# Kernel optimization log

Hardware: AMD Instinct MI355X
Metric: run time of the kernel (lower is better)

## Reference

```python
import jax, jax.numpy as jnp
import numpy as np

B, T, C, H = 2, 2048, 1024, 16
D = C // H  # head dim = 64


def setup_inputs() -> dict:
    key = jax.random.key(0)
    ks = jax.random.split(key, 9)
    x = jax.random.normal(ks[0], (B, T, C), dtype=jnp.float32)
    # causal mask: True above the diagonal => positions to mask out
    mask = jnp.triu(jnp.ones((T, T), dtype=bool), k=1)[None, None]  # [1,1,T,T]
    s = 0.02
    Wq = jax.random.normal(ks[1], (C, C), dtype=jnp.float32) * s
    Wk = jax.random.normal(ks[2], (C, C), dtype=jnp.float32) * s
    Wv = jax.random.normal(ks[3], (C, C), dtype=jnp.float32) * s
    Wo = jax.random.normal(ks[4], (C, C), dtype=jnp.float32) * s
    bq = jax.random.normal(ks[5], (C,), dtype=jnp.float32) * s
    bk = jax.random.normal(ks[6], (C,), dtype=jnp.float32) * s
    bv = jax.random.normal(ks[7], (C,), dtype=jnp.float32) * s
    bo = jax.random.normal(ks[8], (C,), dtype=jnp.float32) * s
    return {"x": x, "mask": mask, "Wq": Wq, "bq": bq, "Wk": Wk, "bk": bk,
            "Wv": Wv, "bv": bv, "Wo": Wo, "bo": bo}


def reference(x, mask, Wq, bq, Wk, bk, Wv, bv, Wo, bo):
    b, t, c = x.shape
    # QKV projections, split heads -> [B,H,T,D]
    q = (x @ Wq + bq).reshape(b, t, H, D).transpose(0, 2, 1, 3)
    k = (x @ Wk + bk).reshape(b, t, H, D).transpose(0, 2, 1, 3)
    v = (x @ Wv + bv).reshape(b, t, H, D).transpose(0, 2, 1, 3)
    # scaled dot-product scores [B,H,T,T]
    att = jnp.einsum('bhtd,bhsd->bhts', q, k) * (1.0 / jnp.sqrt(jnp.float32(D)))
    att = jnp.where(mask, jnp.float32(-jnp.inf), att)
    att = jax.nn.softmax(att, axis=-1)  # dropout p=0.0 -> identity
    y = jnp.einsum('bhts,bhsd->bhtd', att, v)  # [B,H,T,D]
    y = y.transpose(0, 2, 1, 3).reshape(b, t, c)
    return y @ Wo + bo
```

## Files before the change

kernel.cpp:

```cpp
#include <hip/hip_runtime.h>
#include <hip/hip_bf16.h>

#define BB 2
#define TT 2048
#define CC 1024
#define HH 16
#define DD 64
#define MM (BB*TT)

typedef float f32x4 __attribute__((ext_vector_type(4)));
typedef __bf16 bf16x8 __attribute__((ext_vector_type(8)));
typedef unsigned int u32x4 __attribute__((ext_vector_type(4)));
typedef unsigned int u32x2 __attribute__((ext_vector_type(2)));

__device__ __forceinline__ unsigned short f2bf(float f) {
    unsigned int u = __float_as_uint(f);
    u += 0x7fff + ((u >> 16) & 1);
    return (unsigned short)(u >> 16);
}
__device__ __forceinline__ unsigned int pk2(float a, float b) {
    return (unsigned int)f2bf(a) | ((unsigned int)f2bf(b) << 16);
}

__global__ __launch_bounds__(256) void cvt_f32_bf16(
    const float* __restrict__ in, unsigned short* __restrict__ out)
{
    const size_t i = (size_t)blockIdx.x * 256 + threadIdx.x;
    const float4* in4 = (const float4*)in;
    float4 a = in4[2 * i], b = in4[2 * i + 1];
    u32x4 o;
    o[0] = pk2(a.x, a.y); o[1] = pk2(a.z, a.w);
    o[2] = pk2(b.x, b.y); o[3] = pk2(b.z, b.w);
    *(u32x4*)(out + 8 * i) = o;
}

__global__ __launch_bounds__(256) void wtrans_kernel(
    const float* __restrict__ W0, const float* __restrict__ W1,
    const float* __restrict__ W2, const float* __restrict__ W3,
    unsigned short* __restrict__ wt)
{
    const int tid = threadIdx.x;
    const int n0 = blockIdx.x * 64;
    const int k0 = blockIdx.y * 64;
    const int which = blockIdx.z;
    const float* W = (which == 0) ? W0 : (which == 1) ? W1 : (which == 2) ? W2 : W3;

    __shared__ float t_lds[64][68];

    #pragma unroll
    for (int p = 0; p < 4; ++p) {
        int idx = tid + p * 256;
        int r   = idx >> 4;
        int c4  = (idx & 15) * 4;
        *(float4*)&t_lds[r][c4] = *(const float4*)(W + (size_t)(k0 + r) * CC + n0 + c4);
    }
    __syncthreads();

    const int nl = tid >> 2;
    const int ks = (tid & 3) * 16;
    unsigned int w[8];
    #pragma unroll
    for (int j = 0; j < 8; ++j)
        w[j] = pk2(t_lds[ks + 2 * j][nl], t_lds[ks + 2 * j + 1][nl]);
    unsigned short* dst = wt + (size_t)which * CC * CC + (size_t)(n0 + nl) * CC + k0 + ks;
    u32x4 o0; o0[0] = w[0]; o0[1] = w[1]; o0[2] = w[2]; o0[3] = w[3];
    u32x4 o1; o1[0] = w[4]; o1[1] = w[5]; o1[2] = w[6]; o1[3] = w[7];
    *(u32x4*)dst = o0;
    *(u32x4*)(dst + 8) = o1;
}

__global__ __launch_bounds__(256) void gemm_qkv_mfma(
    const unsigned short* __restrict__ xbf, const unsigned short* __restrict__ wt,
    const float* __restrict__ bq, const float* __restrict__ bk, const float* __restrict__ bv,
    unsigned short* __restrict__ qbf, unsigned short* __restrict__ kbf,
    unsigned short* __restrict__ vtbf)
{
    const int tid = threadIdx.x;
    const int m0 = blockIdx.y * 128;
    const int nc0 = blockIdx.x * 128;
    const int which = nc0 >> 10;
    const int cb = nc0 & 1023;
    const unsigned short* Bt = wt + (size_t)which * CC * CC;
    const float* bias = (which == 0) ? bq : (which == 1) ? bk : bv;

    __shared__ unsigned short lds_a[128][40];
    __shared__ unsigned short lds_b[128][40];

    const int lane = tid & 63;
    const int wv = tid >> 6;
    const int wm = (wv & 1) * 64;
    const int wn = (wv >> 1) * 64;
    const int fr = lane & 15;
    const int ks = lane >> 4;

    f32x4 acc[4][4];
    #pragma unroll
    for (int i = 0; i < 4; ++i)
        #pragma unroll
        for (int j = 0; j < 4; ++j) { acc[i][j][0]=0.f; acc[i][j][1]=0.f; acc[i][j][2]=0.f; acc[i][j][3]=0.f; }

    for (int k0 = 0; k0 < CC; k0 += 32) {
        __syncthreads();
        #pragma unroll
        for (int p = 0; p < 2; ++p) {
            int c = tid + p * 256;
            int row = c >> 2, slot = c & 3;
            *(u32x4*)&lds_a[row][slot * 8] =
                *(const u32x4*)(xbf + (size_t)(m0 + row) * CC + k0 + slot * 8);
            *(u32x4*)&lds_b[row][slot * 8] =
                *(const u32x4*)(Bt + (size_t)(cb + row) * CC + k0 + slot * 8);
        }
        __syncthreads();

        bf16x8 af[4], bfv[4];
        #pragma unroll
        for (int i = 0; i < 4; ++i) {
            af[i]  = __builtin_bit_cast(bf16x8, *(const u32x4*)&lds_a[wm + i * 16 + fr][ks * 8]);
            bfv[i] = __builtin_bit_cast(bf16x8, *(const u32x4*)&lds_b[wn + i * 16 + fr][ks * 8]);
        }
        #pragma unroll
        for (int mi = 0; mi < 4; ++mi)
            #pragma unroll
            for (int ni = 0; ni < 4; ++ni)
                acc[mi][ni] = __builtin_amdgcn_mfma_f32_16x16x32_bf16(af[mi], bfv[ni], acc[mi][ni], 0, 0, 0);
    }

    #pragma unroll
    for (int ni = 0; ni < 4; ++ni) {
        const int c = cb + wn + ni * 16 + fr;
        const float bv2 = bias[c];
        const int h = c >> 6, d = c & 63;
        #pragma unroll
        for (int mi = 0; mi < 4; ++mi) {
            const int mb = m0 + wm + mi * 16 + ks * 4;
            const int b = mb >> 11, t = mb & 2047;
            if (which == 2) {
                u32x2 pkd;
                pkd[0] = pk2(acc[mi][ni][0] + bv2, acc[mi][ni][1] + bv2);
                pkd[1] = pk2(acc[mi][ni][2] + bv2, acc[mi][ni][3] + bv2);
                *(u32x2*)(vtbf + (((size_t)(b * HH + h) * DD + d) * TT) + t) = pkd;
            } else {
                unsigned short* dst = (which == 0) ? qbf : kbf;
                const float scl = (which == 0) ? 0.125f : 1.0f;
                #pragma unroll
                for (int j = 0; j < 4; ++j)
                    dst[(((size_t)(b * HH + h) * TT + (t + j)) * DD) + d] =
                        f2bf((acc[mi][ni][j] + bv2) * scl);
            }
        }
    }
}

__global__ __launch_bounds__(256) void attn_mfma(
    const unsigned short* __restrict__ qbf, const unsigned short* __restrict__ kbf,
    const unsigned short* __restrict__ vtbf, unsigned short* __restrict__ ybf)
{
    const int tid  = threadIdx.x;
    const int w    = tid >> 6;
    const int lane = tid & 63;
    const int g    = lane >> 4;
    const int i    = lane & 15;
    const int qi   = 31 - (int)blockIdx.x;
    const int h    = blockIdx.y;
    const int b    = blockIdx.z;
    const int q0   = qi * 64;
    const size_t hq = (size_t)(b * HH + h) * TT * DD;
    const size_t hv = (size_t)(b * HH + h) * DD * TT;

    __shared__ __align__(16) unsigned short k_lds[64][72];
    __shared__ __align__(16) unsigned short vt_lds[64][72];
    __shared__ __align__(16) unsigned short p_lds[64][72];

    bf16x8 qf[2];
    {
        const unsigned short* qrow = qbf + hq + (size_t)(q0 + 16 * w + i) * DD + g * 8;
        qf[0] = __builtin_bit_cast(bf16x8, *(const u32x4*)qrow);
        qf[1] = __builtin_bit_cast(bf16x8, *(const u32x4*)(qrow + 32));
    }

    f32x4 o_acc[4];
    f32x4 m_i, l_i;
    #pragma unroll
    for (int ni = 0; ni < 4; ++ni) { o_acc[ni][0]=0.f; o_acc[ni][1]=0.f; o_acc[ni][2]=0.f; o_acc[ni][3]=0.f; }
    #pragma unroll
    for (int e = 0; e < 4; ++e) { m_i[e] = -1e30f; l_i[e] = 0.f; }

    for (int kk = 0; kk <= qi; ++kk) {
        const int s0 = kk * 64;
        __syncthreads();
        #pragma unroll
        for (int p = 0; p < 2; ++p) {
            int c = tid + p * 256;
            int row = c >> 3, slot = c & 7;
            *(u32x4*)&k_lds[row][slot * 8] =
                *(const u32x4*)(kbf + hq + (size_t)(s0 + row) * DD + slot * 8);
            *(u32x4*)&vt_lds[row][slot * 8] =
                *(const u32x4*)(vtbf + hv + (size_t)row * TT + s0 + slot * 8);
        }
        __syncthreads();

        f32x4 s_acc[4];
        #pragma unroll
        for (int ni = 0; ni < 4; ++ni) { s_acc[ni][0]=0.f; s_acc[ni][1]=0.f; s_acc[ni][2]=0.f; s_acc[ni][3]=0.f; }
        #pragma unroll
        for (int ks = 0; ks < 2; ++ks)
            #pragma unroll
            for (int ni = 0; ni < 4; ++ni) {
                bf16x8 kb = __builtin_bit_cast(bf16x8,
                    *(const u32x4*)&k_lds[ni * 16 + i][ks * 32 + g * 8]);
                s_acc[ni] = __builtin_amdgcn_mfma_f32_16x16x32_bf16(qf[ks], kb, s_acc[ni], 0, 0, 0);
            }

        if (kk == qi) {
            #pragma unroll
            for (int ni = 0; ni < 4; ++ni)
                #pragma unroll
                for (int reg = 0; reg < 4; ++reg)
                    if (ni * 16 + i > 16 * w + 4 * g + reg) s_acc[ni][reg] = -1e30f;
        }

        f32x4 rmax = s_acc[0];
        #pragma unroll
        for (int ni = 1; ni < 4; ++ni)
            #pragma unroll
            for (int e = 0; e < 4; ++e) rmax[e] = fmaxf(rmax[e], s_acc[ni][e]);
        #pragma unroll
        for (int msk = 1; msk < 16; msk <<= 1)
            #pragma unroll
            for (int e = 0; e < 4; ++e) rmax[e] = fmaxf(rmax[e], __shfl_xor(rmax[e], msk));

        f32x4 m_new, alpha;
        #pragma unroll
        for (int e = 0; e < 4; ++e) {
            m_new[e] = fmaxf(m_i[e], rmax[e]);
            alpha[e] = __expf(m_i[e] - m_new[e]);
        }
        f32x4 rsum;
        #pragma unroll
        for (int e = 0; e < 4; ++e) rsum[e] = 0.f;
        #pragma unroll
        for (int ni = 0; ni < 4; ++ni)
            #pragma unroll
            for (int e = 0; e < 4; ++e) {
                float pv = __expf(s_acc[ni][e] - m_new[e]);
                s_acc[ni][e] = pv;
                rsum[e] += pv;
            }
        #pragma unroll
        for (int msk = 1; msk < 16; msk <<= 1)
            #pragma unroll
            for (int e = 0; e < 4; ++e) rsum[e] += __shfl_xor(rsum[e], msk);
        #pragma unroll
        for (int e = 0; e < 4; ++e) {
            l_i[e] = l_i[e] * alpha[e] + rsum[e];
            m_i[e] = m_new[e];
        }
        #pragma unroll
        for (int ni = 0; ni < 4; ++ni)
            #pragma unroll
            for (int e = 0; e < 4; ++e) o_acc[ni][e] *= alpha[e];

        #pragma unroll
        for (int ni = 0; ni < 4; ++ni)
            #pragma unroll
            for (int reg = 0; reg < 4; ++reg)
                p_lds[16 * w + 4 * g + reg][ni * 16 + i] = f2bf(s_acc[ni][reg]);

        #pragma unroll
        for (int ks = 0; ks < 2; ++ks) {
            bf16x8 pa = __builtin_bit_cast(bf16x8,
                *(const u32x4*)&p_lds[16 * w + i][ks * 32 + g * 8]);
            #pragma unroll
            for (int ni = 0; ni < 4; ++ni) {
                bf16x8 vb = __builtin_bit_cast(bf16x8,
                    *(const u32x4*)&vt_lds[ni * 16 + i][ks * 32 + g * 8]);
                o_acc[ni] = __builtin_amdgcn_mfma_f32_16x16x32_bf16(pa, vb, o_acc[ni], 0, 0, 0);
            }
        }
    }

    f32x4 inv;
    #pragma unroll
    for (int e = 0; e < 4; ++e) inv[e] = 1.0f / l_i[e];
    #pragma unroll
    for (int ni = 0; ni < 4; ++ni)
        #pragma unroll
        for (int reg = 0; reg < 4; ++reg)
            ybf[((size_t)b * TT + (q0 + 16 * w + 4 * g + reg)) * CC + h * DD + ni * 16 + i] =
                f2bf(o_acc[ni][reg] * inv[reg]);
}

__global__ __launch_bounds__(256) void gemm_out_mfma(
    const unsigned short* __restrict__ ybf, const unsigned short* __restrict__ wt_o,
    const float* __restrict__ bo, float* __restrict__ out)
{
    const int tid = threadIdx.x;
    const int m0 = blockIdx.y * 128;
    const int n0 = blockIdx.x * 128;

    __shared__ unsigned short lds_a[128][40];
    __shared__ unsigned short lds_b[128][40];

    const int lane = tid & 63;
    const int wv = tid >> 6;
    const int wm = (wv & 1) * 64;
    const int wn = (wv >> 1) * 64;
    const int fr = lane & 15;
    const int ks = lane >> 4;

    f32x4 acc[4][4];
    #pragma unroll
    for (int i = 0; i < 4; ++i)
        #pragma unroll
        for (int j = 0; j < 4; ++j) { acc[i][j][0]=0.f; acc[i][j][1]=0.f; acc[i][j][2]=0.f; acc[i][j][3]=0.f; }

    for (int k0 = 0; k0 < CC; k0 += 32) {
        __syncthreads();
        #pragma unroll
        for (int p = 0; p < 2; ++p) {
            int c = tid + p * 256;
            int row = c >> 2, slot = c & 3;
            *(u32x4*)&lds_a[row][slot * 8] =
                *(const u32x4*)(ybf + (size_t)(m0 + row) * CC + k0 + slot * 8);
            *(u32x4*)&lds_b[row][slot * 8] =
                *(const u32x4*)(wt_o + (size_t)(n0 + row) * CC + k0 + slot * 8);
        }
        __syncthreads();

        bf16x8 af[4], bfv[4];
        #pragma unroll
        for (int i = 0; i < 4; ++i) {
            af[i]  = __builtin_bit_cast(bf16x8, *(const u32x4*)&lds_a[wm + i * 16 + fr][ks * 8]);
            bfv[i] = __builtin_bit_cast(bf16x8, *(const u32x4*)&lds_b[wn + i * 16 + fr][ks * 8]);
        }
        #pragma unroll
        for (int mi = 0; mi < 4; ++mi)
            #pragma unroll
            for (int ni = 0; ni < 4; ++ni)
                acc[mi][ni] = __builtin_amdgcn_mfma_f32_16x16x32_bf16(af[mi], bfv[ni], acc[mi][ni], 0, 0, 0);
    }

    #pragma unroll
    for (int ni = 0; ni < 4; ++ni) {
        const int n = n0 + wn + ni * 16 + fr;
        const float bv2 = bo[n];
        #pragma unroll
        for (int mi = 0; mi < 4; ++mi) {
            #pragma unroll
            for (int j = 0; j < 4; ++j) {
                const int m = m0 + wm + mi * 16 + ks * 4 + j;
                out[(size_t)m * CC + n] = acc[mi][ni][j] + bv2;
            }
        }
    }
}

extern "C" void kernel_launch(void* const* d_in, const int* in_sizes, int n_in,
                              void* d_out, int out_size, void* d_ws, size_t ws_size,
                              hipStream_t stream) {
    const float* x  = (const float*)d_in[0];
    const float* Wq = (const float*)d_in[2];
    const float* bq = (const float*)d_in[3];
    const float* Wk = (const float*)d_in[4];
    const float* bk = (const float*)d_in[5];
    const float* Wv = (const float*)d_in[6];
    const float* bv = (const float*)d_in[7];
    const float* Wo = (const float*)d_in[8];
    const float* bo = (const float*)d_in[9];
    float* out = (float*)d_out;

    const size_t NE = (size_t)MM * CC;
    unsigned short* xbf  = (unsigned short*)d_ws;
    unsigned short* ybf  = xbf + NE;
    unsigned short* wt   = ybf + NE;
    unsigned short* qbf  = wt + (size_t)4 * CC * CC;
    unsigned short* kbf  = qbf + NE;
    unsigned short* vtbf = kbf + NE;

    cvt_f32_bf16<<<2048, 256, 0, stream>>>(x, xbf);
    wtrans_kernel<<<dim3(16, 16, 4), 256, 0, stream>>>(Wq, Wk, Wv, Wo, wt);
    gemm_qkv_mfma<<<dim3(24, 32), 256, 0, stream>>>(
        xbf, wt, bq, bk, bv, qbf, kbf, vtbf);
    attn_mfma<<<dim3(TT / 64, HH, BB), 256, 0, stream>>>(qbf, kbf, vtbf, ybf);
    gemm_out_mfma<<<dim3(8, 32), 256, 0, stream>>>(
        ybf, wt + (size_t)3 * CC * CC, bo, out);
}
```

Baseline: 296.0 us.

## Use direct global-to-LDS loads in GEMMs and 128-row attention tiles with prefetch

Both GEMMs now fill LDS with global_load_lds instead of loading through registers, and drop the padding so each 16-byte row segment is contiguous. This can add LDS bank conflicts on the fragment reads. The attention kernel now runs 512 threads over 128 query rows, so each K/V tile loaded into LDS serves twice as many queries. It also prefetches the next K/V tile into registers while computing the current one, and lets the first four waves skip the final diagonal tile. The larger block and LDS footprint may lower occupancy and leave waves idle on that last tile.

Result: faster. 273.5 us (-7.6%).

```diff
diff --git a/kernel.cpp b/kernel.cpp
--- a/kernel.cpp
+++ b/kernel.cpp
@@ -20,6 +20,13 @@
 }
 __device__ __forceinline__ unsigned int pk2(float a, float b) {
     return (unsigned int)f2bf(a) | ((unsigned int)f2bf(b) << 16);
+}
+
+__device__ __forceinline__ void gload_lds16(const void* g, void* l) {
+    __builtin_amdgcn_global_load_lds(
+        (const __attribute__((address_space(1))) unsigned int*)(unsigned long long)g,
+        (__attribute__((address_space(3))) unsigned int*)(unsigned int)(unsigned long long)l,
+        16, 0, 0);
 }
 
 __global__ __launch_bounds__(256) void cvt_f32_bf16(
@@ -83,8 +90,8 @@
     const unsigned short* Bt = wt + (size_t)which * CC * CC;
     const float* bias = (which == 0) ? bq : (which == 1) ? bk : bv;
 
-    __shared__ unsigned short lds_a[128][40];
-    __shared__ unsigned short lds_b[128][40];
+    __shared__ __align__(16) unsigned short lds_a[128][32];
+    __shared__ __align__(16) unsigned short lds_b[128][32];
 
     const int lane = tid & 63;
     const int wv = tid >> 6;
@@ -93,6 +100,9 @@
     const int fr = lane & 15;
     const int ks = lane >> 4;
 
+    const int lrow = lane >> 2;
+    const int lcol = (lane & 3) * 8;
+
     f32x4 acc[4][4];
     #pragma unroll
     for (int i = 0; i < 4; ++i)
@@ -102,13 +112,10 @@
     for (int k0 = 0; k0 < CC; k0 += 32) {
         __syncthreads();
         #pragma unroll
-        for (int p = 0; p < 2; ++p) {
-            int c = tid + p * 256;
-            int row = c >> 2, slot = c & 3;
-            *(u32x4*)&lds_a[row][slot * 8] =
-                *(const u32x4*)(xbf + (size_t)(m0 + row) * CC + k0 + slot * 8);
-            *(u32x4*)&lds_b[row][slot * 8] =
-                *(const u32x4*)(Bt + (size_t)(cb + row) * CC + k0 + slot * 8);
+        for (int c = 0; c < 2; ++c) {
+            const int r0 = (wv * 2 + c) * 16;
+            gload_lds16(xbf + (size_t)(m0 + r0 + lrow) * CC + k0 + lcol, &lds_a[r0][0]);
+            gload_lds16(Bt  + (size_t)(cb + r0 + lrow) * CC + k0 + lcol, &lds_b[r0][0]);
         }
         __syncthreads();
 
@@ -151,7 +158,7 @@
     }
 }
 
-__global__ __launch_bounds__(256) void attn_mfma(
+__global__ __launch_bounds__(512) void attn_mfma(
     const unsigned short* __restrict__ qbf, const unsigned short* __restrict__ kbf,
     const unsigned short* __restrict__ vtbf, unsigned short* __restrict__ ybf)
 {
@@ -160,16 +167,16 @@
     const int lane = tid & 63;
     const int g    = lane >> 4;
     const int i    = lane & 15;
-    const int qi   = 31 - (int)blockIdx.x;
+    const int qi   = 15 - (int)blockIdx.x;
     const int h    = blockIdx.y;
     const int b    = blockIdx.z;
-    const int q0   = qi * 64;
+    const int q0   = qi * 128;
     const size_t hq = (size_t)(b * HH + h) * TT * DD;
     const size_t hv = (size_t)(b * HH + h) * DD * TT;
 
     __shared__ __align__(16) unsigned short k_lds[64][72];
     __shared__ __align__(16) unsigned short vt_lds[64][72];
-    __shared__ __align__(16) unsigned short p_lds[64][72];
+    __shared__ __align__(16) unsigned short p_lds[128][72];
 
     bf16x8 qf[2];
     {
@@ -185,38 +192,48 @@
     #pragma unroll
     for (int e = 0; e < 4; ++e) { m_i[e] = -1e30f; l_i[e] = 0.f; }
 
-    for (int kk = 0; kk <= qi; ++kk) {
+    const int srow  = tid >> 3;
+    const int sslot = (tid & 7) * 8;
+
+    const int nt = 2 * qi + 2;
+    u32x4 kreg = *(const u32x4*)(kbf + hq + (size_t)srow * DD + sslot);
+    u32x4 vreg = *(const u32x4*)(vtbf + hv + (size_t)srow * TT + sslot);
+
+    for (int kk = 0; kk < nt; ++kk) {
+        __syncthreads();
+        *(u32x4*)&k_lds[srow][sslot]  = kreg;
+        *(u32x4*)&vt_lds[srow][sslot] = vreg;
+        __syncthreads();
+        if (kk + 1 < nt) {
+            const int s1 = (kk + 1) * 64;
+            kreg = *(const u32x4*)(kbf + hq + (size_t)(s1 + srow) * DD + sslot);
+            vreg = *(const u32x4*)(vtbf + hv + (size_t)srow * TT + s1 + sslot);
+        }
+
+        if (kk == nt - 1 && w < 4) continue;
+
         const int s0 = kk * 64;
-        __syncthreads();
-        #pragma unroll
-        for (int p = 0; p < 2; ++p) {
-            int c = tid + p * 256;
-            int row = c >> 3, slot = c & 7;
-            *(u32x4*)&k_lds[row][slot * 8] =
-                *(const u32x4*)(kbf + hq + (size_t)(s0 + row) * DD + slot * 8);
-            *(u32x4*)&vt_lds[row][slot * 8] =
-                *(const u32x4*)(vtbf + hv + (size_t)row * TT + s0 + slot * 8);
-        }
-        __syncthreads();
-
         f32x4 s_acc[4];
         #pragma unroll
         for (int ni = 0; ni < 4; ++ni) { s_acc[ni][0]=0.f; s_acc[ni][1]=0.f; s_acc[ni][2]=0.f; s_acc[ni][3]=0.f; }
         #pragma unroll
-        for (int ks = 0; ks < 2; ++ks)
+        for (int lks = 0; lks < 2; ++lks)
             #pragma unroll
             for (int ni = 0; ni < 4; ++ni) {
                 bf16x8 kb = __builtin_bit_cast(bf16x8,
-                    *(const u32x4*)&k_lds[ni * 16 + i][ks * 32 + g * 8]);
-                s_acc[ni] = __builtin_amdgcn_mfma_f32_16x16x32_bf16(qf[ks], kb, s_acc[ni], 0, 0, 0);
-            }
-
-        if (kk == qi) {
-            #pragma unroll
-            for (int ni = 0; ni < 4; ++ni)
+                    *(const u32x4*)&k_lds[ni * 16 + i][lks * 32 + g * 8]);
+                s_acc[ni] = __builtin_amdgcn_mfma_f32_16x16x32_bf16(qf[lks], kb, s_acc[ni], 0, 0, 0);
+            }
+
+        if (kk >= 2 * qi) {
+            const int r_glob = q0 + 16 * w + 4 * g;
+            #pragma unroll
+            for (int ni = 0; ni < 4; ++ni) {
+                const int s_glob = s0 + ni * 16 + i;
                 #pragma unroll
                 for (int reg = 0; reg < 4; ++reg)
-                    if (ni * 16 + i > 16 * w + 4 * g + reg) s_acc[ni][reg] = -1e30f;
+                    if (s_glob > r_glob + reg) s_acc[ni][reg] = -1e30f;
+            }
         }
 
         f32x4 rmax = s_acc[0];
@@ -267,13 +284,13 @@
                 p_lds[16 * w + 4 * g + reg][ni * 16 + i] = f2bf(s_acc[ni][reg]);
 
         #pragma unroll
-        for (int ks = 0; ks < 2; ++ks) {
+        for (int lks = 0; lks < 2; ++lks) {
             bf16x8 pa = __builtin_bit_cast(bf16x8,
-                *(const u32x4*)&p_lds[16 * w + i][ks * 32 + g * 8]);
+                *(const u32x4*)&p_lds[16 * w + i][lks * 32 + g * 8]);
             #pragma unroll
             for (int ni = 0; ni < 4; ++ni) {
                 bf16x8 vb = __builtin_bit_cast(bf16x8,
-                    *(const u32x4*)&vt_lds[ni * 16 + i][ks * 32 + g * 8]);
+                    *(const u32x4*)&vt_lds[ni * 16 + i][lks * 32 + g * 8]);
                 o_acc[ni] = __builtin_amdgcn_mfma_f32_16x16x32_bf16(pa, vb, o_acc[ni], 0, 0, 0);
             }
         }
@@ -298,8 +315,8 @@
     const int m0 = blockIdx.y * 128;
     const int n0 = blockIdx.x * 128;
 
-    __shared__ unsigned short lds_a[128][40];
-    __shared__ unsigned short lds_b[128][40];
+    __shared__ __align__(16) unsigned short lds_a[128][32];
+    __shared__ __align__(16) unsigned short lds_b[128][32];
 
     const int lane = tid & 63;
     const int wv = tid >> 6;
@@ -307,6 +324,8 @@
     const int wn = (wv >> 1) * 64;
     const int fr = lane & 15;
     const int ks = lane >> 4;
+    const int lrow = lane >> 2;
+    const int lcol = (lane & 3) * 8;
 
     f32x4 acc[4][4];
     #pragma unroll
@@ -317,13 +336,10 @@
     for (int k0 = 0; k0 < CC; k0 += 32) {
         __syncthreads();
         #pragma unroll
-        for (int p = 0; p < 2; ++p) {
-            int c = tid + p * 256;
-            int row = c >> 2, slot = c & 3;
-            *(u32x4*)&lds_a[row][slot * 8] =
-                *(const u32x4*)(ybf + (size_t)(m0 + row) * CC + k0 + slot * 8);
-            *(u32x4*)&lds_b[row][slot * 8] =
-                *(const u32x4*)(wt_o + (size_t)(n0 + row) * CC + k0 + slot * 8);
+        for (int c = 0; c < 2; ++c) {
+            const int r0 = (wv * 2 + c) * 16;
+            gload_lds16(ybf  + (size_t)(m0 + r0 + lrow) * CC + k0 + lcol, &lds_a[r0][0]);
+            gload_lds16(wt_o + (size_t)(n0 + r0 + lrow) * CC + k0 + lcol, &lds_b[r0][0]);
         }
         __syncthreads();
 
@@ -381,7 +397,7 @@
     wtrans_kernel<<<dim3(16, 16, 4), 256, 0, stream>>>(Wq, Wk, Wv, Wo, wt);
     gemm_qkv_mfma<<<dim3(24, 32), 256, 0, stream>>>(
         xbf, wt, bq, bk, bv, qbf, kbf, vtbf);
-    attn_mfma<<<dim3(TT / 64, HH, BB), 256, 0, stream>>>(qbf, kbf, vtbf, ybf);
+    attn_mfma<<<dim3(TT / 128, HH, BB), 512, 0, stream>>>(qbf, kbf, vtbf, ybf);
     gemm_out_mfma<<<dim3(8, 32), 256, 0, stream>>>(
         ybf, wt + (size_t)3 * CC * CC, bo, out);
 }
```
